# Kernel optimization log

Measured on AMD Instinct MI355X. Metric: run time of the kernel, lower is better.

## Reference

```python
import jax, jax.numpy as jnp
import numpy as np

B, T, INPUT_DIM = 4, 2048, 1024
DIM, H = 64, 16  # per-head dim, n_heads


def setup_inputs() -> dict:
    key = jax.random.key(0)
    k1, k2, k3, k4 = jax.random.split(key, 4)
    x = jax.random.normal(k1, (B, T, INPUT_DIM), dtype=jnp.float32)
    # nn.Linear(input_dim, 3*h*d, bias=False)
    w_qkv = jax.random.normal(k2, (INPUT_DIM, 3 * H * DIM), dtype=jnp.float32) * (INPUT_DIM ** -0.5)
    # nn.Linear(h*d, input_dim) with bias
    w_out = jax.random.normal(k3, (H * DIM, INPUT_DIM), dtype=jnp.float32) * ((H * DIM) ** -0.5)
    b_out = jax.random.normal(k4, (INPUT_DIM,), dtype=jnp.float32) * 0.01
    return {"x": x, "w_qkv": w_qkv, "w_out": w_out, "b_out": b_out}


def reference(x, w_qkv, w_out, b_out):
    b, t, _ = x.shape
    scale = DIM ** -0.5
    qkv = x @ w_qkv                                   # [b, t, 3*h*d]
    # 'b t (qkv h d) -> qkv b h t d'
    qkv = qkv.reshape(b, t, 3, H, DIM)
    qkv = jnp.transpose(qkv, (2, 0, 3, 1, 4))         # [3, b, h, t, d]
    q, k, v = qkv[0], qkv[1], qkv[2]
    dot = jnp.einsum('bhtd,bhkd->bhtk', q, k) * scale # [b, h, t, t]
    att = jax.nn.softmax(dot, axis=-1)
    out = jnp.einsum('bhtk,bhkd->bhtd', att, v)       # [b, h, t, d]
    out = jnp.transpose(out, (0, 2, 1, 3)).reshape(b, t, H * DIM)
    return out @ w_out + b_out
```

## Files before the change

### kernel.cpp

```cpp
#include <hip/hip_runtime.h>
#include <hip/hip_bf16.h>
#include <stdint.h>

typedef __attribute__((ext_vector_type(8))) short bf16x8;
typedef __attribute__((ext_vector_type(4))) short s16x4;
typedef __attribute__((ext_vector_type(4))) float f32x4;
typedef __attribute__((ext_vector_type(16))) float f32x16;

__device__ __forceinline__ void mfma_bf16(f32x4& c, bf16x8 a, bf16x8 b) {
  asm("v_mfma_f32_16x16x32_bf16 %0, %1, %2, %0" : "+v"(c) : "v"(a), "v"(b));
}
__device__ __forceinline__ void mfma32_bf16(f32x16& c, bf16x8 a, bf16x8 b) {
  asm("v_mfma_f32_32x32x16_bf16 %0, %1, %2, %0" : "+v"(c) : "v"(a), "v"(b));
}

__device__ __forceinline__ void gload_lds16(const void* g, void* lds) {
  __builtin_amdgcn_global_load_lds(
      (const __attribute__((address_space(1))) void*)g,
      (__attribute__((address_space(3))) void*)lds, 16, 0, 0);
}

__global__ void cvt_f32_bf16(const float* __restrict__ in, __hip_bfloat16* __restrict__ out, int n4) {
  int i = blockIdx.x * blockDim.x + threadIdx.x;
  if (i >= n4) return;
  float4 v = reinterpret_cast<const float4*>(in)[i];
  __hip_bfloat162 a = __float22bfloat162_rn(make_float2(v.x, v.y));
  __hip_bfloat162 b = __float22bfloat162_rn(make_float2(v.z, v.w));
  reinterpret_cast<__hip_bfloat162*>(out)[i * 2]     = a;
  reinterpret_cast<__hip_bfloat162*>(out)[i * 2 + 1] = b;
}

__global__ void transpose_cvt(const float* __restrict__ in, __hip_bfloat16* __restrict__ out,
                              int R, int C) {
  __shared__ float tile[32][33];
  int c0 = blockIdx.x * 32, r0 = blockIdx.y * 32;
#pragma unroll
  for (int k = 0; k < 4; k++)
    tile[threadIdx.y + 8 * k][threadIdx.x] =
        in[(size_t)(r0 + threadIdx.y + 8 * k) * C + c0 + threadIdx.x];
  __syncthreads();
#pragma unroll
  for (int k = 0; k < 4; k++)
    out[(size_t)(c0 + threadIdx.y + 8 * k) * R + r0 + threadIdx.x] =
        __float2bfloat16(tile[threadIdx.x][threadIdx.y + 8 * k]);
}

template <int MODE>
__global__ __launch_bounds__(256) void gemm_bf16(
    const __hip_bfloat16* __restrict__ A, const __hip_bfloat16* __restrict__ Bt,
    int M, int N, int K,
    __hip_bfloat16* __restrict__ qb, __hip_bfloat16* __restrict__ kb,
    __hip_bfloat16* __restrict__ vt,
    float* __restrict__ outp, const float* __restrict__ bias) {
  constexpr int BK = 32;
  __shared__ __align__(16) __hip_bfloat16 As[128 * BK];
  __shared__ __align__(16) __hip_bfloat16 Bs[128 * BK];
  const int tid = threadIdx.x;
  const int wave = tid >> 6, lane = tid & 63;
  const int wr = wave >> 1, wc = wave & 1;
  const int m0 = blockIdx.y * 128;
  const int n0 = (MODE == 2 ? 2048 : 0) + blockIdx.x * 128;

  f32x4 acc[4][4];
#pragma unroll
  for (int i = 0; i < 4; i++)
#pragma unroll
    for (int j = 0; j < 4; j++) acc[i][j] = (f32x4)(0.0f);

  const int c0 = wave * 2, c1 = c0 + 1;
  const int srow0 = c0 * 16 + (lane >> 2);
  const int srow1 = c1 * 16 + (lane >> 2);
  const int scol = (lane & 3) * 8;
  const __hip_bfloat16* Ag0 = A + (size_t)(m0 + srow0) * K + scol;
  const __hip_bfloat16* Ag1 = A + (size_t)(m0 + srow1) * K + scol;
  const __hip_bfloat16* Bg0 = Bt + (size_t)(n0 + srow0) * K + scol;
  const __hip_bfloat16* Bg1 = Bt + (size_t)(n0 + srow1) * K + scol;
  __hip_bfloat16* AsP0 = &As[c0 * 512];
  __hip_bfloat16* AsP1 = &As[c1 * 512];
  __hip_bfloat16* BsP0 = &Bs[c0 * 512];
  __hip_bfloat16* BsP1 = &Bs[c1 * 512];

  for (int kk = 0; kk < K; kk += BK) {
    gload_lds16(Ag0 + kk, AsP0);
    gload_lds16(Ag1 + kk, AsP1);
    gload_lds16(Bg0 + kk, BsP0);
    gload_lds16(Bg1 + kk, BsP1);
    __syncthreads();
    bf16x8 af[4], bfr[4];
#pragma unroll
    for (int i = 0; i < 4; i++)
      af[i] = *(const bf16x8*)&As[(wr * 64 + i * 16 + (lane & 15)) * BK + (lane >> 4) * 8];
#pragma unroll
    for (int j = 0; j < 4; j++)
      bfr[j] = *(const bf16x8*)&Bs[(wc * 64 + j * 16 + (lane & 15)) * BK + (lane >> 4) * 8];
#pragma unroll
    for (int i = 0; i < 4; i++)
#pragma unroll
      for (int j = 0; j < 4; j++) {
        if constexpr (MODE == 2)
          mfma_bf16(acc[i][j], bfr[j], af[i]);
        else
          mfma_bf16(acc[i][j], af[i], bfr[j]);
      }
    __syncthreads();
  }

  if constexpr (MODE == 0) {
#pragma unroll
    for (int j = 0; j < 4; j++) {
      int col = n0 + wc * 64 + j * 16 + (lane & 15);
      int sel = col >> 10;
      int h = (col >> 6) & 15;
      int d = col & 63;
      __hip_bfloat16* dst = sel ? kb : qb;
      float scl = sel ? 1.0f : 0.18033688f;
#pragma unroll
      for (int i = 0; i < 4; i++) {
#pragma unroll
        for (int r = 0; r < 4; r++) {
          int row = m0 + wr * 64 + i * 16 + (lane >> 4) * 4 + r;
          int b = row >> 11, t = row & 2047;
          dst[(((size_t)b * 16 + h) * 2048 + t) * 64 + d] = __float2bfloat16(acc[i][j][r] * scl);
        }
      }
    }
  } else if constexpr (MODE == 2) {
#pragma unroll
    for (int j = 0; j < 4; j++) {
#pragma unroll
      for (int r = 0; r < 4; r++) {
        int nrow = n0 + wc * 64 + j * 16 + (lane >> 4) * 4 + r;
        int h = (nrow >> 6) & 15;
        int d = nrow & 63;
#pragma unroll
        for (int i = 0; i < 4; i++) {
          int tcol = m0 + wr * 64 + i * 16 + (lane & 15);
          int b = tcol >> 11, t = tcol & 2047;
          vt[(((size_t)b * 16 + h) * 64 + d) * 2048 + t] = __float2bfloat16(acc[i][j][r]);
        }
      }
    }
  } else {
#pragma unroll
    for (int j = 0; j < 4; j++) {
      int col = n0 + wc * 64 + j * 16 + (lane & 15);
      float bv = bias[col];
#pragma unroll
      for (int i = 0; i < 4; i++) {
#pragma unroll
        for (int r = 0; r < 4; r++) {
          int row = m0 + wr * 64 + i * 16 + (lane >> 4) * 4 + r;
          outp[(size_t)row * N + col] = acc[i][j][r] + bv;
        }
      }
    }
  }
}

__global__ __launch_bounds__(512, 4) void attn_fwd(
    const __hip_bfloat16* __restrict__ Qb, const __hip_bfloat16* __restrict__ Kb,
    const __hip_bfloat16* __restrict__ Vtg, __hip_bfloat16* __restrict__ Ob) {
  constexpr int T = 2048;
  constexpr float THR = 11.5f;
  __shared__ __align__(16) __hip_bfloat16 Ks[2][4096];
  __shared__ __align__(16) __hip_bfloat16 Vs[2][4096];
  const int tid = threadIdx.x, wave = tid >> 6, lane = tid & 63;

  int id = ((int)blockIdx.x & 7) * 64 + ((int)blockIdx.x >> 3);
  const int bh = id >> 3, q0 = (id & 7) * 256;
  const size_t baseQ = (size_t)bh * T * 64;
  const size_t baseV = (size_t)bh * 64 * T;
  const int l31 = lane & 31, half = lane >> 5;

  bf16x8 qf[4];
  const int qrow = q0 + wave * 32 + l31;
#pragma unroll
  for (int ks = 0; ks < 4; ks++)
    qf[ks] = *(const bf16x8*)&Qb[baseQ + (size_t)qrow * 64 + ks * 16 + half * 8];

  float m_run = 0.0f;
  float l_part = 0.0f;
  f32x16 o0 = (f32x16)(0.0f), o1 = (f32x16)(0.0f);

  const int sr = lane >> 3;
  const int q8 = (lane & 7) ^ sr;
  const char* KgB = (const char*)(Kb + baseQ);
  const char* VgB = (const char*)(Vtg + baseV);
  const int swz = (l31 & 7) << 4;

#define STAGE(kt, buf)                                                                          \
  do {                                                                                          \
    char* kd = (char*)Ks[buf];                                                                  \
    char* vd = (char*)Vs[buf];                                                                  \
    gload_lds16(KgB + (size_t)((kt) * 64 + wave * 8 + sr) * 128 + q8 * 16, kd + wave * 1024);   \
    gload_lds16(VgB + (size_t)(wave * 8 + sr) * 4096 + (kt) * 128 + q8 * 16, vd + wave * 1024); \
  } while (0)

  STAGE(0, 0);
  int cur = 0;

  for (int kt = 0; kt < T / 64; kt++) {
    if (kt < T / 64 - 1) {
      STAGE(kt + 1, cur ^ 1);
      asm volatile("s_waitcnt vmcnt(2)" ::: "memory");
    } else {
      asm volatile("s_waitcnt vmcnt(0)" ::: "memory");
    }
    __builtin_amdgcn_s_barrier();
    __builtin_amdgcn_sched_barrier(0);
    const char* KsB = (const char*)Ks[cur];
    const char* VtB = (const char*)Vs[cur];

    f32x16 s0, s1;
#pragma unroll
    for (int r = 0; r < 16; r++) {
      s0[r] = -m_run;
      s1[r] = -m_run;
    }
    __builtin_amdgcn_s_setprio(1);
#pragma unroll
    for (int ks = 0; ks < 4; ks++) {
      bf16x8 kf0 = *(const bf16x8*)(KsB + ((l31 * 128 + ks * 32 + half * 16) ^ swz));
      bf16x8 kf1 = *(const bf16x8*)(KsB + (((32 + l31) * 128 + ks * 32 + half * 16) ^ swz));
      mfma32_bf16(s0, kf0, qf[ks]);
      mfma32_bf16(s1, kf1, qf[ks]);
    }
    __builtin_amdgcn_s_setprio(0);

    float mx[8];
#pragma unroll
    for (int i = 0; i < 8; i++)
      mx[i] = fmaxf(fmaxf(s0[2 * i], s0[2 * i + 1]), fmaxf(s1[2 * i], s1[2 * i + 1]));
    float tm = fmaxf(fmaxf(fmaxf(mx[0], mx[1]), fmaxf(mx[2], mx[3])),
                     fmaxf(fmaxf(mx[4], mx[5]), fmaxf(mx[6], mx[7])));
    tm = fmaxf(tm, __shfl_xor(tm, 32));

    if (!__all(tm <= THR)) {
      float d = fmaxf(tm, 0.0f);
      float alpha = __builtin_exp2f(-d);
      m_run += d;
      l_part *= alpha;
#pragma unroll
      for (int r = 0; r < 16; r++) {
        s0[r] -= d;
        s1[r] -= d;
        o0[r] *= alpha;
        o1[r] *= alpha;
      }
    }

    float rs0 = 0.0f, rs1 = 0.0f;
#pragma unroll
    for (int r = 0; r < 16; r++) {
      s0[r] = __builtin_exp2f(s0[r]);
      s1[r] = __builtin_exp2f(s1[r]);
      rs0 += s0[r];
      rs1 += s1[r];
    }
    l_part += rs0 + rs1;

    __builtin_amdgcn_s_setprio(1);
#pragma unroll
    for (int kb = 0; kb < 2; kb++) {
      int cw[8];
#pragma unroll
      for (int m = 0; m < 8; m++) {
        float pa = (kb == 0) ? s0[2 * m] : s1[2 * m];
        float pb = (kb == 0) ? s0[2 * m + 1] : s1[2 * m + 1];
        __hip_bfloat162 h2 = __float22bfloat162_rn(make_float2(pa, pb));
        cw[m] = *(int*)&h2;
      }
      asm("v_permlane32_swap_b32 %0, %1" : "+v"(cw[0]), "+v"(cw[2]));
      asm("v_permlane32_swap_b32 %0, %1" : "+v"(cw[1]), "+v"(cw[3]));
      asm("v_permlane32_swap_b32 %0, %1" : "+v"(cw[4]), "+v"(cw[6]));
      asm("v_permlane32_swap_b32 %0, %1" : "+v"(cw[5]), "+v"(cw[7]));
      int4 w0 = make_int4(cw[0], cw[1], cw[2], cw[3]);
      int4 w1 = make_int4(cw[4], cw[5], cw[6], cw[7]);
      bf16x8 pb0 = *(bf16x8*)&w0;
      bf16x8 pb1 = *(bf16x8*)&w1;
      bf16x8 va0 = *(const bf16x8*)(VtB + ((l31 * 128 + kb * 64 + half * 16) ^ swz));
      bf16x8 vb0 = *(const bf16x8*)(VtB + (((32 + l31) * 128 + kb * 64 + half * 16) ^ swz));
      bf16x8 va1 = *(const bf16x8*)(VtB + ((l31 * 128 + kb * 64 + 32 + half * 16) ^ swz));
      bf16x8 vb1 = *(const bf16x8*)(VtB + (((32 + l31) * 128 + kb * 64 + 32 + half * 16) ^ swz));
      mfma32_bf16(o0, va0, pb0);
      mfma32_bf16(o1, vb0, pb0);
      mfma32_bf16(o0, va1, pb1);
      mfma32_bf16(o1, vb1, pb1);
    }
    __builtin_amdgcn_s_setprio(0);
    __builtin_amdgcn_sched_barrier(0);
    __builtin_amdgcn_s_barrier();
    cur ^= 1;
  }
#undef STAGE

  float l_run = l_part + __shfl_xor(l_part, 32);
  float inv = 1.0f / l_run;
  const int b = bh >> 4, h = bh & 15;
  const int trow = q0 + wave * 32 + l31;
  __hip_bfloat16* orow = Ob + ((size_t)(b * 2048 + trow)) * 1024 + h * 64;
#pragma unroll
  for (int db = 0; db < 2; db++) {
#pragma unroll
    for (int rq = 0; rq < 4; rq++) {
      int d0 = db * 32 + rq * 8 + half * 4;
      s16x4 w;
#pragma unroll
      for (int e = 0; e < 4; e++) {
        float val = (db == 0 ? o0[rq * 4 + e] : o1[rq * 4 + e]) * inv;
        w[e] = (short)__bfloat16_as_short(__float2bfloat16(val));
      }
      *(s16x4*)(orow + d0) = w;
    }
  }
}

extern "C" void kernel_launch(void* const* d_in, const int* in_sizes, int n_in,
                              void* d_out, int out_size, void* d_ws, size_t ws_size,
                              hipStream_t stream) {
  const float* x = (const float*)d_in[0];
  const float* w_qkv = (const float*)d_in[1];
  const float* w_out = (const float*)d_in[2];
  const float* b_out = (const float*)d_in[3];
  float* out = (float*)d_out;

  size_t need = (size_t)37748736 * 2;
  if (ws_size < need) return;
  __hip_bfloat16* wsp = (__hip_bfloat16*)d_ws;
  __hip_bfloat16* x_bf = wsp;
  __hip_bfloat16* wqkv_t = x_bf + 8192 * 1024;
  __hip_bfloat16* wout_t = wqkv_t + 3072 * 1024;
  __hip_bfloat16* qb = wout_t + 1024 * 1024;
  __hip_bfloat16* kb = qb + 8388608;
  __hip_bfloat16* vt = kb + 8388608;
  __hip_bfloat16* ab = x_bf;

  cvt_f32_bf16<<<8192, 256, 0, stream>>>(x, x_bf, 8192 * 1024 / 4);
  transpose_cvt<<<dim3(3072 / 32, 1024 / 32), dim3(32, 8), 0, stream>>>(w_qkv, wqkv_t, 1024, 3072);
  transpose_cvt<<<dim3(1024 / 32, 1024 / 32), dim3(32, 8), 0, stream>>>(w_out, wout_t, 1024, 1024);
  gemm_bf16<0><<<dim3(16, 64), 256, 0, stream>>>(x_bf, wqkv_t, 8192, 3072, 1024,
                                                 qb, kb, nullptr, nullptr, nullptr);
  gemm_bf16<2><<<dim3(8, 64), 256, 0, stream>>>(x_bf, wqkv_t, 8192, 3072, 1024,
                                                nullptr, nullptr, vt, nullptr, nullptr);
  attn_fwd<<<512, 512, 0, stream>>>(qb, kb, vt, ab);
  gemm_bf16<1><<<dim3(8, 64), 256, 0, stream>>>(ab, wout_t, 8192, 1024, 1024,
                                                nullptr, nullptr, nullptr, out, b_out);
}
```

Baseline: 236.3 us.

## Software-pipeline attention loop with triple-buffered K/V and QK lookahead

```diff
diff --git a/kernel.cpp b/kernel.cpp
--- a/kernel.cpp
+++ b/kernel.cpp
@@ -160,10 +160,10 @@
 __global__ __launch_bounds__(512, 4) void attn_fwd(
     const __hip_bfloat16* __restrict__ Qb, const __hip_bfloat16* __restrict__ Kb,
     const __hip_bfloat16* __restrict__ Vtg, __hip_bfloat16* __restrict__ Ob) {
-  constexpr int T = 2048;
+  constexpr int T = 2048, NT = T / 64;
   constexpr float THR = 11.5f;
-  __shared__ __align__(16) __hip_bfloat16 Ks[2][4096];
-  __shared__ __align__(16) __hip_bfloat16 Vs[2][4096];
+  __shared__ __align__(16) __hip_bfloat16 Ks[3][4096];
+  __shared__ __align__(16) __hip_bfloat16 Vs[3][4096];
   const int tid = threadIdx.x, wave = tid >> 6, lane = tid & 63;
 
   int id = ((int)blockIdx.x & 7) * 64 + ((int)blockIdx.x >> 3);
@@ -181,6 +181,8 @@
   float m_run = 0.0f;
   float l_part = 0.0f;
   f32x16 o0 = (f32x16)(0.0f), o1 = (f32x16)(0.0f);
+  f32x16 s0, s1;
+  bf16x8 pA0, pA1, pB0, pB1;
 
   const int sr = lane >> 3;
   const int q8 = (lane & 7) ^ sr;
@@ -188,111 +190,122 @@
   const char* VgB = (const char*)(Vtg + baseV);
   const int swz = (l31 & 7) << 4;
 
-#define STAGE(kt, buf)                                                                          \
-  do {                                                                                          \
-    char* kd = (char*)Ks[buf];                                                                  \
-    char* vd = (char*)Vs[buf];                                                                  \
-    gload_lds16(KgB + (size_t)((kt) * 64 + wave * 8 + sr) * 128 + q8 * 16, kd + wave * 1024);   \
-    gload_lds16(VgB + (size_t)(wave * 8 + sr) * 4096 + (kt) * 128 + q8 * 16, vd + wave * 1024); \
+#define STAGE(kt, buf)                                                                            \
+  do {                                                                                            \
+    gload_lds16(KgB + (size_t)((kt) * 64 + wave * 8 + sr) * 128 + q8 * 16,                        \
+                (char*)Ks[buf] + wave * 1024);                                                    \
+    gload_lds16(VgB + (size_t)(wave * 8 + sr) * 4096 + (kt) * 128 + q8 * 16,                      \
+                (char*)Vs[buf] + wave * 1024);                                                    \
   } while (0)
 
+#define QK_TILE(buf)                                                                              \
+  do {                                                                                            \
+    const char* KsB_ = (const char*)Ks[buf];                                                      \
+    _Pragma("unroll") for (int r = 0; r < 16; r++) { s0[r] = -m_run; s1[r] = -m_run; }            \
+    __builtin_amdgcn_s_setprio(1);                                                                \
+    _Pragma("unroll") for (int ks = 0; ks < 4; ks++) {                                            \
+      bf16x8 kf0 = *(const bf16x8*)(KsB_ + ((l31 * 128 + ks * 32 + half * 16) ^ swz));            \
+      bf16x8 kf1 = *(const bf16x8*)(KsB_ + (((32 + l31) * 128 + ks * 32 + half * 16) ^ swz));     \
+      mfma32_bf16(s0, kf0, qf[ks]);                                                               \
+      mfma32_bf16(s1, kf1, qf[ks]);                                                               \
+    }                                                                                             \
+    __builtin_amdgcn_s_setprio(0);                                                                \
+  } while (0)
+
+#define SMAX_PACK()                                                                               \
+  do {                                                                                            \
+    float mx[8];                                                                                  \
+    _Pragma("unroll") for (int i = 0; i < 8; i++)                                                 \
+        mx[i] = fmaxf(fmaxf(s0[2 * i], s0[2 * i + 1]), fmaxf(s1[2 * i], s1[2 * i + 1]));          \
+    float tm = fmaxf(fmaxf(fmaxf(mx[0], mx[1]), fmaxf(mx[2], mx[3])),                             \
+                     fmaxf(fmaxf(mx[4], mx[5]), fmaxf(mx[6], mx[7])));                            \
+    tm = fmaxf(tm, __shfl_xor(tm, 32));                                                           \
+    if (!__all(tm <= THR)) {                                                                      \
+      float d = fmaxf(tm, 0.0f);                                                                  \
+      float alpha = __builtin_exp2f(-d);                                                          \
+      m_run += d;                                                                                 \
+      l_part *= alpha;                                                                            \
+      _Pragma("unroll") for (int r = 0; r < 16; r++) {                                            \
+        s0[r] -= d; s1[r] -= d; o0[r] *= alpha; o1[r] *= alpha;                                   \
+      }                                                                                           \
+    }                                                                                             \
+    float rs0 = 0.0f, rs1 = 0.0f;                                                                 \
+    _Pragma("unroll") for (int r = 0; r < 16; r++) {                                              \
+      s0[r] = __builtin_exp2f(s0[r]);                                                             \
+      s1[r] = __builtin_exp2f(s1[r]);                                                             \
+      rs0 += s0[r]; rs1 += s1[r];                                                                 \
+    }                                                                                             \
+    l_part += rs0 + rs1;                                                                          \
+    int cw[8];                                                                                    \
+    _Pragma("unroll") for (int m = 0; m < 8; m++) {                                               \
+      __hip_bfloat162 h2 = __float22bfloat162_rn(make_float2(s0[2 * m], s0[2 * m + 1]));          \
+      cw[m] = *(int*)&h2;                                                                         \
+    }                                                                                             \
+    asm("v_permlane32_swap_b32 %0, %1" : "+v"(cw[0]), "+v"(cw[2]));                               \
+    asm("v_permlane32_swap_b32 %0, %1" : "+v"(cw[1]), "+v"(cw[3]));                               \
+    asm("v_permlane32_swap_b32 %0, %1" : "+v"(cw[4]), "+v"(cw[6]));                               \
+    asm("v_permlane32_swap_b32 %0, %1" : "+v"(cw[5]), "+v"(cw[7]));                               \
+    { int4 w0 = make_int4(cw[0], cw[1], cw[2], cw[3]); pA0 = *(bf16x8*)&w0; }                     \
+    { int4 w1 = make_int4(cw[4], cw[5], cw[6], cw[7]); pA1 = *(bf16x8*)&w1; }                     \
+    _Pragma("unroll") for (int m = 0; m < 8; m++) {                                               \
+      __hip_bfloat162 h2 = __float22bfloat162_rn(make_float2(s1[2 * m], s1[2 * m + 1]));          \
+      cw[m] = *(int*)&h2;                                                                         \
+    }                                                                                             \
+    asm("v_permlane32_swap_b32 %0, %1" : "+v"(cw[0]), "+v"(cw[2]));                               \
+    asm("v_permlane32_swap_b32 %0, %1" : "+v"(cw[1]), "+v"(cw[3]));                               \
+    asm("v_permlane32_swap_b32 %0, %1" : "+v"(cw[4]), "+v"(cw[6]));                               \
+    asm("v_permlane32_swap_b32 %0, %1" : "+v"(cw[5]), "+v"(cw[7]));                               \
+    { int4 w0 = make_int4(cw[0], cw[1], cw[2], cw[3]); pB0 = *(bf16x8*)&w0; }                     \
+    { int4 w1 = make_int4(cw[4], cw[5], cw[6], cw[7]); pB1 = *(bf16x8*)&w1; }                     \
+  } while (0)
+
+#define PV_TILE(buf)                                                                              \
+  do {                                                                                            \
+    const char* VtB_ = (const char*)Vs[buf];                                                      \
+    __builtin_amdgcn_s_setprio(1);                                                                \
+    _Pragma("unroll") for (int kb = 0; kb < 2; kb++) {                                            \
+      bf16x8 p0 = kb ? pB0 : pA0;                                                                 \
+      bf16x8 p1 = kb ? pB1 : pA1;                                                                 \
+      bf16x8 va0 = *(const bf16x8*)(VtB_ + ((l31 * 128 + kb * 64 + half * 16) ^ swz));            \
+      bf16x8 vb0 = *(const bf16x8*)(VtB_ + (((32 + l31) * 128 + kb * 64 + half * 16) ^ swz));     \
+      bf16x8 va1 = *(const bf16x8*)(VtB_ + ((l31 * 128 + kb * 64 + 32 + half * 16) ^ swz));       \
+      bf16x8 vb1 = *(const bf16x8*)(VtB_ + (((32 + l31) * 128 + kb * 64 + 32 + half * 16) ^ swz));\
+      mfma32_bf16(o0, va0, p0);                                                                   \
+      mfma32_bf16(o1, vb0, p0);                                                                   \
+      mfma32_bf16(o0, va1, p1);                                                                   \
+      mfma32_bf16(o1, vb1, p1);                                                                   \
+    }                                                                                             \
+    __builtin_amdgcn_s_setprio(0);                                                                \
+  } while (0)
+
   STAGE(0, 0);
-  int cur = 0;
-
-  for (int kt = 0; kt < T / 64; kt++) {
-    if (kt < T / 64 - 1) {
-      STAGE(kt + 1, cur ^ 1);
+  STAGE(1, 1);
+  asm volatile("s_waitcnt vmcnt(2)" ::: "memory");
+  __builtin_amdgcn_s_barrier();
+  __builtin_amdgcn_sched_barrier(0);
+  QK_TILE(0);
+
+  int cA = 0, cB = 1, cC = 2;
+  for (int t = 0; t < NT - 1; ++t) {
+    if (t + 2 < NT) STAGE(t + 2, cC);
+    SMAX_PACK();
+    PV_TILE(cA);
+    if (t < NT - 2)
       asm volatile("s_waitcnt vmcnt(2)" ::: "memory");
-    } else {
+    else
       asm volatile("s_waitcnt vmcnt(0)" ::: "memory");
-    }
     __builtin_amdgcn_s_barrier();
     __builtin_amdgcn_sched_barrier(0);
-    const char* KsB = (const char*)Ks[cur];
-    const char* VtB = (const char*)Vs[cur];
-
-    f32x16 s0, s1;
-#pragma unroll
-    for (int r = 0; r < 16; r++) {
-      s0[r] = -m_run;
-      s1[r] = -m_run;
-    }
-    __builtin_amdgcn_s_setprio(1);
-#pragma unroll
-    for (int ks = 0; ks < 4; ks++) {
-      bf16x8 kf0 = *(const bf16x8*)(KsB + ((l31 * 128 + ks * 32 + half * 16) ^ swz));
-      bf16x8 kf1 = *(const bf16x8*)(KsB + (((32 + l31) * 128 + ks * 32 + half * 16) ^ swz));
-      mfma32_bf16(s0, kf0, qf[ks]);
-      mfma32_bf16(s1, kf1, qf[ks]);
-    }
-    __builtin_amdgcn_s_setprio(0);
-
-    float mx[8];
-#pragma unroll
-    for (int i = 0; i < 8; i++)
-      mx[i] = fmaxf(fmaxf(s0[2 * i], s0[2 * i + 1]), fmaxf(s1[2 * i], s1[2 * i + 1]));
-    float tm = fmaxf(fmaxf(fmaxf(mx[0], mx[1]), fmaxf(mx[2], mx[3])),
-                     fmaxf(fmaxf(mx[4], mx[5]), fmaxf(mx[6], mx[7])));
-    tm = fmaxf(tm, __shfl_xor(tm, 32));
-
-    if (!__all(tm <= THR)) {
-      float d = fmaxf(tm, 0.0f);
-      float alpha = __builtin_exp2f(-d);
-      m_run += d;
-      l_part *= alpha;
-#pragma unroll
-      for (int r = 0; r < 16; r++) {
-        s0[r] -= d;
-        s1[r] -= d;
-        o0[r] *= alpha;
-        o1[r] *= alpha;
-      }
-    }
-
-    float rs0 = 0.0f, rs1 = 0.0f;
-#pragma unroll
-    for (int r = 0; r < 16; r++) {
-      s0[r] = __builtin_exp2f(s0[r]);
-      s1[r] = __builtin_exp2f(s1[r]);
-      rs0 += s0[r];
-      rs1 += s1[r];
-    }
-    l_part += rs0 + rs1;
-
-    __builtin_amdgcn_s_setprio(1);
-#pragma unroll
-    for (int kb = 0; kb < 2; kb++) {
-      int cw[8];
-#pragma unroll
-      for (int m = 0; m < 8; m++) {
-        float pa = (kb == 0) ? s0[2 * m] : s1[2 * m];
-        float pb = (kb == 0) ? s0[2 * m + 1] : s1[2 * m + 1];
-        __hip_bfloat162 h2 = __float22bfloat162_rn(make_float2(pa, pb));
-        cw[m] = *(int*)&h2;
-      }
-      asm("v_permlane32_swap_b32 %0, %1" : "+v"(cw[0]), "+v"(cw[2]));
-      asm("v_permlane32_swap_b32 %0, %1" : "+v"(cw[1]), "+v"(cw[3]));
-      asm("v_permlane32_swap_b32 %0, %1" : "+v"(cw[4]), "+v"(cw[6]));
-      asm("v_permlane32_swap_b32 %0, %1" : "+v"(cw[5]), "+v"(cw[7]));
-      int4 w0 = make_int4(cw[0], cw[1], cw[2], cw[3]);
-      int4 w1 = make_int4(cw[4], cw[5], cw[6], cw[7]);
-      bf16x8 pb0 = *(bf16x8*)&w0;
-      bf16x8 pb1 = *(bf16x8*)&w1;
-      bf16x8 va0 = *(const bf16x8*)(VtB + ((l31 * 128 + kb * 64 + half * 16) ^ swz));
-      bf16x8 vb0 = *(const bf16x8*)(VtB + (((32 + l31) * 128 + kb * 64 + half * 16) ^ swz));
-      bf16x8 va1 = *(const bf16x8*)(VtB + ((l31 * 128 + kb * 64 + 32 + half * 16) ^ swz));
-      bf16x8 vb1 = *(const bf16x8*)(VtB + (((32 + l31) * 128 + kb * 64 + 32 + half * 16) ^ swz));
-      mfma32_bf16(o0, va0, pb0);
-      mfma32_bf16(o1, vb0, pb0);
-      mfma32_bf16(o0, va1, pb1);
-      mfma32_bf16(o1, vb1, pb1);
-    }
-    __builtin_amdgcn_s_setprio(0);
-    __builtin_amdgcn_sched_barrier(0);
-    __builtin_amdgcn_s_barrier();
-    cur ^= 1;
+    QK_TILE(cB);
+    int tmp = cA; cA = cB; cB = cC; cC = tmp;
   }
+  SMAX_PACK();
+  PV_TILE(cA);
+
 #undef STAGE
+#undef QK_TILE
+#undef SMAX_PACK
+#undef PV_TILE
 
   float l_run = l_part + __shfl_xor(l_part, 32);
   float inv = 1.0f / l_run;
```

New measurement: 236.5 us. Within noise of the previous version (+0.1%).
